# Performance work log

Hardware: AMD Instinct MI355X
Metric: run time of the kernel (lower is better)

The kernel has to match this reference:

```python
import jax, jax.numpy as jnp
import numpy as np

N_WRD = 2000
WCODE = 3
EMB = 32
VSIZE = 7
VIEW = (16, 16)
B = 64
CSIZE = 128


def _vcode():
    # torch.meshgrid with default 'ij' indexing, cat -> (2, H*W) -> (H*W, 2)
    x = jnp.linspace(-1.0, 1.0, VIEW[0])
    y = jnp.linspace(-1.0, 1.0, VIEW[1])
    xg, yg = jnp.meshgrid(x, y, indexing='ij')
    return jnp.stack([xg.reshape(-1), yg.reshape(-1)], axis=-1)  # (V, 2)


def setup_inputs() -> dict:
    key = jax.random.key(0)
    ks = jax.random.split(key, 20)
    s = 0.02
    d = {
        'view_cell': jax.random.normal(ks[0], (B, CSIZE, VIEW[0] * VIEW[1]), jnp.float32),
        'v': jax.random.normal(ks[1], (B, VSIZE), jnp.float32),
        'w2c_w1': jax.random.normal(ks[2], (VSIZE, 512), jnp.float32) * s,
        'w2c_b1': jnp.zeros((512,), jnp.float32),
        'w2c_w2': jax.random.normal(ks[3], (512, WCODE * N_WRD), jnp.float32) * s,
        'w2c_b2': jnp.zeros((WCODE * N_WRD,), jnp.float32),
        'fc1_w': jax.random.normal(ks[4], (WCODE, 256), jnp.float32) * s,
        'fc1_b': jnp.zeros((256,), jnp.float32),
        'fc2_w': jax.random.normal(ks[5], (256, 256), jnp.float32) * s,
        'fc2_b': jnp.zeros((256,), jnp.float32),
        'fca_w': jax.random.normal(ks[6], (256, 1), jnp.float32) * s,
        'fca_b': jnp.zeros((1,), jnp.float32),
        'fce_w': jax.random.normal(ks[7], (256, EMB), jnp.float32) * s,
        'fce_b': jnp.zeros((EMB,), jnp.float32),
        'vse_w1': jax.random.normal(ks[8], (2, 128), jnp.float32) * s,
        'vse_b1': jnp.zeros((128,), jnp.float32),
        'vse_w2': jax.random.normal(ks[9], (128, EMB), jnp.float32) * s,
        'vse_b2': jnp.zeros((EMB,), jnp.float32),
    }
    return d


def reference(view_cell, v, w2c_w1, w2c_b1, w2c_w2, w2c_b2,
              fc1_w, fc1_b, fc2_w, fc2_b, fca_w, fca_b, fce_w, fce_b,
              vse_w1, vse_b1, vse_w2, vse_b2):
    b = v.shape[0]
    # w2c: v -> per-cell world codes
    h0 = jax.nn.relu(v @ w2c_w1 + w2c_b1)                     # (B, 512)
    wcode = (h0 @ w2c_w2 + w2c_b2).reshape(-1, WCODE)          # (B*N, 3)
    h = jax.nn.relu(wcode @ fc1_w + fc1_b)                     # (B*N, 256)
    h = jax.nn.relu(h @ fc2_w + fc2_b)
    activation = jax.nn.sigmoid(h @ fca_w + fca_b).reshape(b, N_WRD, 1)
    cs_emb = (h @ fce_w + fce_b).reshape(b, N_WRD, EMB)        # (B, N, E)
    # view-space embedding of the pixel grid
    vcode = _vcode()                                           # (V, 2)
    vs = jax.nn.relu(vcode @ vse_w1 + vse_b1) @ vse_w2 + vse_b2  # (V, E)
    # relation / gated softmax routing
    relation = jnp.einsum('bne,ve->bnv', cs_emb, vs)           # (B, N, V)
    route = jax.nn.softmax(relation, axis=2) * activation      # (B, N, V)
    # write: view_cell (B, C, V) @ route^T (B, V, N) -> (B, C, N)
    wrd_cell = jnp.einsum('bcv,bnv->bcn', view_cell, route)
    return wrd_cell
```

## Files before the change

### kernel.cpp

```cpp
#include <hip/hip_runtime.h>
#include <hip/hip_bf16.h>
#include <math.h>

#define NWRD 2000

typedef __attribute__((ext_vector_type(8)))  short short8;
typedef __attribute__((ext_vector_type(16))) float f32x16;

#define WS_FC2WT 0
#define WS_WCODE (WS_FC2WT + 32768)
#define WS_VSB   (WS_WCODE + 384000)
#define WS_W2T   (WS_VSB + 4096)
#define WS_VCB   (WS_W2T + 1536000)
#define WS_FCEWT (WS_VCB + 1048576)
#define WS_H0B   (WS_FCEWT + 4096)
#define WS_FCAWB (WS_H0B + 16384)

__device__ __forceinline__ unsigned short f2bf(float x) {
    unsigned int u = __float_as_uint(x);
    u += 0x7fffu + ((u >> 16) & 1u);
    return (unsigned short)(u >> 16);
}
__device__ __forceinline__ unsigned int pkbf(float lo, float hi) {
    unsigned int r;
    asm("v_cvt_pk_bf16_f32 %0, %1, %2" : "=v"(r) : "v"(lo), "v"(hi));
    return r;
}

#define PR_K2  94
#define PR_VCB (PR_K2 + 1024)
#define PR_VSB (PR_VCB + 32)
#define PR_FC2 (PR_VSB + 16)
#define PREP_N (PR_FC2 + 1)
__global__ __launch_bounds__(256) void kprep(
        const float* __restrict__ vc, unsigned short* __restrict__ vcb,
        const float* __restrict__ w2,
        const float* __restrict__ v, const float* __restrict__ w1,
        const float* __restrict__ b1, const float* __restrict__ b2,
        float* __restrict__ wcode,
        const float* __restrict__ vse_w1, const float* __restrict__ vse_b1,
        const float* __restrict__ vse_w2, const float* __restrict__ vse_b2,
        unsigned short* __restrict__ vsb,
        const float* __restrict__ fc2_w, unsigned short* __restrict__ fc2wT,
        const float* __restrict__ fce_w, unsigned short* __restrict__ fcewT,
        const float* __restrict__ fca_w, unsigned short* __restrict__ fcawB) {
    __shared__ __align__(16) unsigned short smem[10240];
    int bid = blockIdx.x, t = threadIdx.x;
    if (bid < PR_K2) {
        unsigned short* ha = smem;
        unsigned short* wb = smem + 4608;
        int n0 = bid * 64;
        int w = t >> 6, lane = t & 63, l31 = lane & 31, h = lane >> 5;
        int mt = w & 1, nt = w >> 1;
        int kk = t & 63, mg = t >> 6;
        int colc = n0 + kk; if (colc > 5999) colc = 5999;
        f32x16 acc;
#pragma unroll
        for (int i = 0; i < 16; i++) acc[i] = 0.f;
        for (int p = 0; p < 8; p++) {
            int k0 = p * 64;
            float w1c[7];
#pragma unroll
            for (int q = 0; q < 7; q++) w1c[q] = w1[q*512 + k0 + kk];
            float bbv = b1[k0 + kk];
#pragma unroll
            for (int mm = 0; mm < 16; mm++) {
                int m = mg*16 + mm;
                float s = bbv;
#pragma unroll
                for (int q = 0; q < 7; q++) s = fmaf(v[m*7 + q], w1c[q], s);
                ha[m*72 + kk] = f2bf(fmaxf(s, 0.f));
            }
#pragma unroll
            for (int i = 0; i < 16; i++)
                wb[kk*72 + mg*16 + i] = f2bf(w2[(size_t)(k0 + mg*16 + i)*6000 + colc]);
            __syncthreads();
#pragma unroll
            for (int ks = 0; ks < 4; ks++) {
                short8 af = *(const short8*)(ha + (mt*32 + l31)*72 + ks*16 + h*8);
                short8 bf = *(const short8*)(wb + (nt*32 + l31)*72 + ks*16 + h*8);
                acc = __builtin_amdgcn_mfma_f32_32x32x16_bf16(af, bf, acc, 0, 0, 0);
            }
            __syncthreads();
        }
        int n = n0 + nt*32 + l31;
        if (n < 6000) {
            float bias = b2[n];
#pragma unroll
            for (int i = 0; i < 16; i++) {
                int row = (i & 3) + 8*(i >> 2) + 4*h;
                wcode[(size_t)(mt*32 + row)*6000 + n] = acc[i] + bias;
            }
        }
    } else if (bid < PR_VCB) {
        int i = ((bid - PR_K2) * 256 + t) * 8;
        float4 f0 = *(const float4*)(vc + i);
        float4 f1 = *(const float4*)(vc + i + 4);
        union { short8 v8; unsigned int u[4]; } o;
        o.u[0] = pkbf(f0.x, f0.y); o.u[1] = pkbf(f0.z, f0.w);
        o.u[2] = pkbf(f1.x, f1.y); o.u[3] = pkbf(f1.z, f1.w);
        *(short8*)(vcb + i) = o.v8;
    } else if (bid < PR_VSB) {
        float* hs = (float*)smem;
        int blk = bid - PR_VCB;
        int m = t & 127, half = t >> 7;
#pragma unroll
        for (int q = 0; q < 4; q++) {
            int vloc = half*4 + q;
            int vv = blk*8 + vloc;
            float x = (2.f/15.f)*(float)(vv >> 4) - 1.f;
            float y = (2.f/15.f)*(float)(vv & 15) - 1.f;
            float hh = vse_b1[m] + x*vse_w1[m] + y*vse_w1[128 + m];
            hs[vloc*128 + m] = fmaxf(hh, 0.f);
        }
        __syncthreads();
        int vloc = t >> 5, e = t & 31;
        float s = vse_b2[e];
        for (int mm = 0; mm < 128; mm++) s = fmaf(hs[vloc*128 + mm], vse_w2[mm*32 + e], s);
        vsb[(blk*8 + vloc)*32 + e] = f2bf(s);
    } else if (bid < PR_FC2) {
        unsigned short (*tile)[72] = (unsigned short(*)[72])smem;
        int b2t = bid - PR_VSB;
        int k0t = (b2t >> 2) * 64, n0t = (b2t & 3) * 64;
        int nl = t & 63, kb = (t >> 6) * 16;
#pragma unroll
        for (int i = 0; i < 16; i++)
            tile[kb + i][nl] = f2bf(fc2_w[(size_t)(k0t + kb + i)*256 + n0t + nl]);
        __syncthreads();
        int kl = t & 63, nb = (t >> 6) * 16;
#pragma unroll
        for (int i = 0; i < 16; i++)
            fc2wT[(size_t)(n0t + nb + i)*256 + k0t + kl] = tile[kl][nb + i];
    } else {
        int e = t & 31, kb = (t >> 5) * 32;
        unsigned short tmp[32];
#pragma unroll
        for (int i = 0; i < 32; i++) tmp[i] = f2bf(fce_w[(size_t)(kb + i)*32 + e]);
#pragma unroll
        for (int i = 0; i < 4; i++)
            *(short8*)(fcewT + (size_t)e*256 + kb + i*8) = *(short8*)(tmp + i*8);
#pragma unroll
        for (int i = 0; i < 32; i++)
            fcawB[(size_t)e*256 + kb + i] = (e == 0) ? f2bf(fca_w[kb + i]) : (unsigned short)0;
    }
}

#define K45_LDS 40192
__global__ __launch_bounds__(512, 4) void k45(
        const unsigned short* __restrict__ vcb,
        const float* __restrict__ wcode,
        const float* __restrict__ fc1_w, const float* __restrict__ fc1_b,
        const unsigned short* __restrict__ fc2wT, const float* __restrict__ fc2_b,
        const float* __restrict__ fca_b_p,
        const unsigned short* __restrict__ fcawB,
        const unsigned short* __restrict__ fcewT, const float* __restrict__ fce_b,
        const unsigned short* __restrict__ vsb,
        float* __restrict__ out) {
    extern __shared__ char lds[];
    unsigned short* buf   = (unsigned short*)lds;
    unsigned short* embL  = (unsigned short*)(lds + 33792);
    float* redS   = (float*)(lds + 38912);
    float* actL   = (float*)(lds + 39936);
    int t = threadIdx.x;
    int w = t >> 6, lane = t & 63, l31 = lane & 31, h = lane >> 5;
    int b = blockIdx.y;
    int n0 = blockIdx.x * 64;

    int jq = (t & 63) * 4;
    int mtF = w & 1, nqF = w >> 1;
    int colA = nqF*64 + l31, colB = colA + 32;
    float baA = fc2_b[colA], baB = fc2_b[colB];
    float be = fce_b[l31];
    float fcab = fca_b_p[0];
    int ntR = w & 1, vq = w >> 1;
    int cq = w >> 1, ntE = w & 1;
    size_t arowE = ((size_t)(b*128 + cq*32 + l31))*256;

    {
        float4 wa  = *(const float4*)(fc1_w + jq);
        float4 wb4 = *(const float4*)(fc1_w + 256 + jq);
        float4 wc  = *(const float4*)(fc1_w + 512 + jq);
        float4 bb4 = *(const float4*)(fc1_b + jq);
        const float* wrow = wcode + (size_t)b*6000;
#pragma unroll
        for (int rr = 0; rr < 8; rr++) {
            int r = w*8 + rr;
            int i = (n0 + r)*3; if (i > 5997) i = 5997;
            float c0 = wrow[i], c1 = wrow[i+1], c2 = wrow[i+2];
            float v0 = fmaxf(fmaf(c2, wc.x, fmaf(c1, wb4.x, fmaf(c0, wa.x, bb4.x))), 0.f);
            float v1 = fmaxf(fmaf(c2, wc.y, fmaf(c1, wb4.y, fmaf(c0, wa.y, bb4.y))), 0.f);
            float v2 = fmaxf(fmaf(c2, wc.z, fmaf(c1, wb4.z, fmaf(c0, wa.z, bb4.z))), 0.f);
            float v3 = fmaxf(fmaf(c2, wc.w, fmaf(c1, wb4.w, fmaf(c0, wa.w, bb4.w))), 0.f);
            uint2 p;
            p.x = pkbf(v0, v1);
            p.y = pkbf(v2, v3);
            *(uint2*)(buf + r*264 + jq) = p;
        }
    }
    __syncthreads();
    f32x16 c0a, c1a;
#pragma unroll
    for (int i = 0; i < 16; i++) { c0a[i] = 0.f; c1a[i] = 0.f; }
#pragma unroll 4
    for (int ks = 0; ks < 16; ks++) {
        int k0 = ks*16 + h*8;
        short8 af  = *(const short8*)(buf + (mtF*32 + l31)*264 + k0);
        short8 bf0 = *(const short8*)(fc2wT + (size_t)colA*256 + k0);
        short8 bf1 = *(const short8*)(fc2wT + (size_t)colB*256 + k0);
        c0a = __builtin_amdgcn_mfma_f32_32x32x16_bf16(af, bf0, c0a, 0, 0, 0);
        c1a = __builtin_amdgcn_mfma_f32_32x32x16_bf16(af, bf1, c1a, 0, 0, 0);
    }
    __syncthreads();
#pragma unroll
    for (int i = 0; i < 16; i++) {
        int row = (i & 3) + 8*(i >> 2) + 4*h;
        unsigned int pk = pkbf(fmaxf(c0a[i] + baA, 0.f), fmaxf(c1a[i] + baB, 0.f));
        buf[(mtF*32 + row)*264 + colA] = (unsigned short)pk;
        buf[(mtF*32 + row)*264 + colB] = (unsigned short)(pk >> 16);
    }
    __syncthreads();
    if (w < 2) {
        f32x16 ce;
#pragma unroll
        for (int i = 0; i < 16; i++) ce[i] = 0.f;
#pragma unroll 4
        for (int ks = 0; ks < 16; ks++) {
            int k0 = ks*16 + h*8;
            short8 af = *(const short8*)(buf + (w*32 + l31)*264 + k0);
            short8 bf = *(const short8*)(fcewT + (size_t)l31*256 + k0);
            ce = __builtin_amdgcn_mfma_f32_32x32x16_bf16(af, bf, ce, 0, 0, 0);
        }
#pragma unroll
        for (int i = 0; i < 16; i += 2) {
            int row = (i & 3) + 8*(i >> 2) + 4*h;
            unsigned int pk = pkbf(ce[i] + be, ce[i+1] + be);
            embL[(w*32 + row)*40 + l31]     = (unsigned short)pk;
            embL[(w*32 + row + 1)*40 + l31] = (unsigned short)(pk >> 16);
        }
    } else if (w < 4) {
        int m = w - 2;
        f32x16 ca;
#pragma unroll
        for (int i = 0; i < 16; i++) ca[i] = 0.f;
#pragma unroll 4
        for (int ks = 0; ks < 16; ks++) {
            int k0 = ks*16 + h*8;
            short8 af = *(const short8*)(buf + (m*32 + l31)*264 + k0);
            short8 bf = *(const short8*)(fcawB + (size_t)l31*256 + k0);
            ca = __builtin_amdgcn_mfma_f32_32x32x16_bf16(af, bf, ca, 0, 0, 0);
        }
        if (l31 == 0) {
#pragma unroll
            for (int i = 0; i < 16; i++) {
                int row = (i & 3) + 8*(i >> 2) + 4*h;
                actL[m*32 + row] = ca[i];
            }
        }
    }
    __syncthreads();
    {
        int nloc = ntR*32 + l31;
        f32x16 ra[2];
#pragma unroll
        for (int mt = 0; mt < 2; mt++)
#pragma unroll
            for (int i = 0; i < 16; i++) ra[mt][i] = 0.f;
#pragma unroll
        for (int s = 0; s < 2; s++) {
            short8 bfrag = *(const short8*)(embL + nloc*40 + s*16 + h*8);
#pragma unroll
            for (int mt = 0; mt < 2; mt++) {
                int vrow = (vq*2 + mt)*32 + l31;
                short8 afrag = *(const short8*)(vsb + vrow*32 + s*16 + h*8);
                ra[mt] = __builtin_amdgcn_mfma_f32_32x32x16_bf16(afrag, bfrag, ra[mt], 0, 0, 0);
            }
        }
        float sm = 0.f;
#pragma unroll
        for (int mt = 0; mt < 2; mt++)
#pragma unroll
            for (int i = 0; i < 16; i++) {
                float e = __expf(ra[mt][i]);
                ra[mt][i] = e;
                sm += e;
            }
        sm += __shfl_xor(sm, 32);
        if (lane < 32) redS[w*32 + l31] = sm;
#pragma unroll
        for (int mt = 0; mt < 2; mt++) {
#pragma unroll
            for (int g = 0; g < 4; g++) {
                int vb = (vq*2 + mt)*32 + 8*g + 4*h;
                unsigned int p0 = pkbf(ra[mt][g*4+0], ra[mt][g*4+1]);
                unsigned int p1 = pkbf(ra[mt][g*4+2], ra[mt][g*4+3]);
                *(uint2*)(buf + nloc*264 + vb) = make_uint2(p0, p1);
            }
        }
    }
    __syncthreads();
    {
        f32x16 cc;
#pragma unroll
        for (int i = 0; i < 16; i++) cc[i] = 0.f;
        const unsigned short* rrow = buf + (ntE*32 + l31)*264;
#pragma unroll 4
        for (int ks = 0; ks < 16; ks++) {
            int k0 = ks*16 + h*8;
            short8 bf = *(const short8*)(rrow + k0);
            short8 a0 = *(const short8*)(vcb + arowE + k0);
            cc = __builtin_amdgcn_mfma_f32_32x32x16_bf16(a0, bf, cc, 0, 0, 0);
        }
        int wloc = ntE*32 + l31;
        float smt = 0.f;
#pragma unroll
        for (int q = 0; q < 4; q++) smt += redS[(q*2 + ntE)*32 + l31];
        float al = actL[wloc] + fcab;
        float scale = (1.f / (1.f + __expf(-al))) / smt;
        int ng = n0 + wloc;
        if (ng < NWRD) {
            float* ob = out + (size_t)b*128*NWRD + ng;
#pragma unroll
            for (int i = 0; i < 16; i++) {
                int crow = (i & 3) + 8*(i >> 2) + 4*h;
                __builtin_nontemporal_store(cc[i]*scale,
                                            ob + (size_t)(cq*32 + crow)*NWRD);
            }
        }
    }
}

extern "C" void kernel_launch(void* const* d_in, const int* in_sizes, int n_in,
                              void* d_out, int out_size, void* d_ws, size_t ws_size,
                              hipStream_t stream) {
    const float* view_cell = (const float*)d_in[0];
    const float* v       = (const float*)d_in[1];
    const float* w2c_w1  = (const float*)d_in[2];
    const float* w2c_b1  = (const float*)d_in[3];
    const float* w2c_w2  = (const float*)d_in[4];
    const float* w2c_b2  = (const float*)d_in[5];
    const float* fc1_w   = (const float*)d_in[6];
    const float* fc1_b   = (const float*)d_in[7];
    const float* fc2_w   = (const float*)d_in[8];
    const float* fc2_b   = (const float*)d_in[9];
    const float* fca_w   = (const float*)d_in[10];
    const float* fca_b   = (const float*)d_in[11];
    const float* fce_w   = (const float*)d_in[12];
    const float* fce_b   = (const float*)d_in[13];
    const float* vse_w1  = (const float*)d_in[14];
    const float* vse_b1  = (const float*)d_in[15];
    const float* vse_w2  = (const float*)d_in[16];
    const float* vse_b2  = (const float*)d_in[17];
    float* ws    = (float*)d_ws;
    unsigned short* fc2wT = (unsigned short*)(ws + WS_FC2WT);
    float* wcode = ws + WS_WCODE;
    unsigned short* vsb   = (unsigned short*)(ws + WS_VSB);
    unsigned short* vcb   = (unsigned short*)(ws + WS_VCB);
    unsigned short* fcewT = (unsigned short*)(ws + WS_FCEWT);
    unsigned short* fcawB = (unsigned short*)(ws + WS_FCAWB);
    float* out   = (float*)d_out;

    kprep<<<PREP_N, 256, 0, stream>>>(view_cell, vcb,
                                      w2c_w2, v, w2c_w1, w2c_b1, w2c_b2, wcode,
                                      vse_w1, vse_b1, vse_w2, vse_b2, vsb,
                                      fc2_w, fc2wT, fce_w, fcewT, fca_w, fcawB);
    (void)hipFuncSetAttribute((const void*)k45,
                              hipFuncAttributeMaxDynamicSharedMemorySize, K45_LDS);
    dim3 g45(32, 64);
    k45<<<g45, 512, K45_LDS, stream>>>(vcb, wcode, fc1_w, fc1_b, fc2wT, fc2_b,
                                       fca_b, fcawB, fcewT, fce_b, vsb, out);
}
```

Before: 235.1 us.

## Double-buffer prep GEMM staging and double k45 block size with 16x16 MFMA splits

The prep w2c GEMM now double-buffers its LDS staging tiles, so the next k-chunk is produced while MFMAs run on the current one. The main fused kernel goes from 512 to 1024 threads per block. Each wave takes a smaller slice of fc2, the embedding/activation heads, the relation softmax and the final write GEMM, with several stages moved to 16x16x32 MFMA tiles. The intent is more waves for latency hiding and better MFMA parallelism in stages that were serialised on a few waves. The cost is a larger prep LDS footprint, a bigger block that may lower occupancy, and more partial-sum reductions for the softmax denominator.

```diff
diff --git a/kernel.cpp b/kernel.cpp
--- a/kernel.cpp
+++ b/kernel.cpp
@@ -6,6 +6,7 @@
 
 typedef __attribute__((ext_vector_type(8)))  short short8;
 typedef __attribute__((ext_vector_type(16))) float f32x16;
+typedef __attribute__((ext_vector_type(4)))  float f32x4v;
 
 #define WS_FC2WT 0
 #define WS_WCODE (WS_FC2WT + 32768)
@@ -44,11 +45,9 @@
         const float* __restrict__ fc2_w, unsigned short* __restrict__ fc2wT,
         const float* __restrict__ fce_w, unsigned short* __restrict__ fcewT,
         const float* __restrict__ fca_w, unsigned short* __restrict__ fcawB) {
-    __shared__ __align__(16) unsigned short smem[10240];
+    __shared__ __align__(16) unsigned short smem[18432];
     int bid = blockIdx.x, t = threadIdx.x;
     if (bid < PR_K2) {
-        unsigned short* ha = smem;
-        unsigned short* wb = smem + 4608;
         int n0 = bid * 64;
         int w = t >> 6, lane = t & 63, l31 = lane & 31, h = lane >> 5;
         int mt = w & 1, nt = w >> 1;
@@ -57,32 +56,42 @@
         f32x16 acc;
 #pragma unroll
         for (int i = 0; i < 16; i++) acc[i] = 0.f;
+#define PRODUCE(p, sel) { \
+        unsigned short* ha = smem + (sel)*9216; \
+        unsigned short* wb = ha + 4608; \
+        int k0 = (p)*64; \
+        float w1c[7]; \
+        _Pragma("unroll") \
+        for (int q = 0; q < 7; q++) w1c[q] = w1[q*512 + k0 + kk]; \
+        float bbv = b1[k0 + kk]; \
+        _Pragma("unroll") \
+        for (int mm = 0; mm < 16; mm++) { \
+            int m = mg*16 + mm; \
+            float s = bbv; \
+            _Pragma("unroll") \
+            for (int q = 0; q < 7; q++) s = fmaf(v[m*7 + q], w1c[q], s); \
+            ha[m*72 + kk] = f2bf(fmaxf(s, 0.f)); \
+        } \
+        _Pragma("unroll") \
+        for (int i = 0; i < 16; i++) \
+            wb[kk*72 + mg*16 + i] = f2bf(w2[(size_t)(k0 + mg*16 + i)*6000 + colc]); }
+        PRODUCE(0, 0)
+        __syncthreads();
         for (int p = 0; p < 8; p++) {
-            int k0 = p * 64;
-            float w1c[7];
-#pragma unroll
-            for (int q = 0; q < 7; q++) w1c[q] = w1[q*512 + k0 + kk];
-            float bbv = b1[k0 + kk];
-#pragma unroll
-            for (int mm = 0; mm < 16; mm++) {
-                int m = mg*16 + mm;
-                float s = bbv;
-#pragma unroll
-                for (int q = 0; q < 7; q++) s = fmaf(v[m*7 + q], w1c[q], s);
-                ha[m*72 + kk] = f2bf(fmaxf(s, 0.f));
-            }
-#pragma unroll
-            for (int i = 0; i < 16; i++)
-                wb[kk*72 + mg*16 + i] = f2bf(w2[(size_t)(k0 + mg*16 + i)*6000 + colc]);
-            __syncthreads();
-#pragma unroll
-            for (int ks = 0; ks < 4; ks++) {
-                short8 af = *(const short8*)(ha + (mt*32 + l31)*72 + ks*16 + h*8);
-                short8 bf = *(const short8*)(wb + (nt*32 + l31)*72 + ks*16 + h*8);
-                acc = __builtin_amdgcn_mfma_f32_32x32x16_bf16(af, bf, acc, 0, 0, 0);
+            if (p < 7) PRODUCE(p + 1, (p + 1) & 1)
+            {
+                unsigned short* ha = smem + (p & 1)*9216;
+                unsigned short* wb = ha + 4608;
+#pragma unroll
+                for (int ks = 0; ks < 4; ks++) {
+                    short8 af = *(const short8*)(ha + (mt*32 + l31)*72 + ks*16 + h*8);
+                    short8 bf = *(const short8*)(wb + (nt*32 + l31)*72 + ks*16 + h*8);
+                    acc = __builtin_amdgcn_mfma_f32_32x32x16_bf16(af, bf, acc, 0, 0, 0);
+                }
             }
             __syncthreads();
         }
+#undef PRODUCE
         int n = n0 + nt*32 + l31;
         if (n < 6000) {
             float bias = b2[n];
@@ -145,8 +154,8 @@
     }
 }
 
-#define K45_LDS 40192
-__global__ __launch_bounds__(512, 4) void k45(
+#define K45_LDS 41216
+__global__ __launch_bounds__(1024, 8) void k45(
         const unsigned short* __restrict__ vcb,
         const float* __restrict__ wcode,
         const float* __restrict__ fc1_w, const float* __restrict__ fc1_b,
@@ -160,31 +169,23 @@
     unsigned short* buf   = (unsigned short*)lds;
     unsigned short* embL  = (unsigned short*)(lds + 33792);
     float* redS   = (float*)(lds + 38912);
-    float* actL   = (float*)(lds + 39936);
+    float* actL   = (float*)(lds + 40960);
     int t = threadIdx.x;
     int w = t >> 6, lane = t & 63, l31 = lane & 31, h = lane >> 5;
+    int l15 = lane & 15, hq = lane >> 4;
     int b = blockIdx.y;
     int n0 = blockIdx.x * 64;
 
-    int jq = (t & 63) * 4;
-    int mtF = w & 1, nqF = w >> 1;
-    int colA = nqF*64 + l31, colB = colA + 32;
-    float baA = fc2_b[colA], baB = fc2_b[colB];
-    float be = fce_b[l31];
-    float fcab = fca_b_p[0];
-    int ntR = w & 1, vq = w >> 1;
-    int cq = w >> 1, ntE = w & 1;
-    size_t arowE = ((size_t)(b*128 + cq*32 + l31))*256;
-
     {
+        int jq = lane * 4;
         float4 wa  = *(const float4*)(fc1_w + jq);
         float4 wb4 = *(const float4*)(fc1_w + 256 + jq);
         float4 wc  = *(const float4*)(fc1_w + 512 + jq);
         float4 bb4 = *(const float4*)(fc1_b + jq);
         const float* wrow = wcode + (size_t)b*6000;
 #pragma unroll
-        for (int rr = 0; rr < 8; rr++) {
-            int r = w*8 + rr;
+        for (int rr = 0; rr < 4; rr++) {
+            int r = w*4 + rr;
             int i = (n0 + r)*3; if (i > 5997) i = 5997;
             float c0 = wrow[i], c1 = wrow[i+1], c2 = wrow[i+2];
             float v0 = fmaxf(fmaf(c2, wc.x, fmaf(c1, wb4.x, fmaf(c0, wa.x, bb4.x))), 0.f);
@@ -198,132 +199,136 @@
         }
     }
     __syncthreads();
-    f32x16 c0a, c1a;
-#pragma unroll
-    for (int i = 0; i < 16; i++) { c0a[i] = 0.f; c1a[i] = 0.f; }
-#pragma unroll 4
-    for (int ks = 0; ks < 16; ks++) {
-        int k0 = ks*16 + h*8;
-        short8 af  = *(const short8*)(buf + (mtF*32 + l31)*264 + k0);
-        short8 bf0 = *(const short8*)(fc2wT + (size_t)colA*256 + k0);
-        short8 bf1 = *(const short8*)(fc2wT + (size_t)colB*256 + k0);
-        c0a = __builtin_amdgcn_mfma_f32_32x32x16_bf16(af, bf0, c0a, 0, 0, 0);
-        c1a = __builtin_amdgcn_mfma_f32_32x32x16_bf16(af, bf1, c1a, 0, 0, 0);
-    }
-    __syncthreads();
-#pragma unroll
-    for (int i = 0; i < 16; i++) {
-        int row = (i & 3) + 8*(i >> 2) + 4*h;
-        unsigned int pk = pkbf(fmaxf(c0a[i] + baA, 0.f), fmaxf(c1a[i] + baB, 0.f));
-        buf[(mtF*32 + row)*264 + colA] = (unsigned short)pk;
-        buf[(mtF*32 + row)*264 + colB] = (unsigned short)(pk >> 16);
-    }
-    __syncthreads();
-    if (w < 2) {
-        f32x16 ce;
-#pragma unroll
-        for (int i = 0; i < 16; i++) ce[i] = 0.f;
+    {
+        int mtF = w & 1;
+        int colF = (w >> 1)*32 + l31;
+        f32x16 acc;
+#pragma unroll
+        for (int i = 0; i < 16; i++) acc[i] = 0.f;
 #pragma unroll 4
         for (int ks = 0; ks < 16; ks++) {
             int k0 = ks*16 + h*8;
-            short8 af = *(const short8*)(buf + (w*32 + l31)*264 + k0);
-            short8 bf = *(const short8*)(fcewT + (size_t)l31*256 + k0);
-            ce = __builtin_amdgcn_mfma_f32_32x32x16_bf16(af, bf, ce, 0, 0, 0);
-        }
-#pragma unroll
-        for (int i = 0; i < 16; i += 2) {
+            short8 af = *(const short8*)(buf + (mtF*32 + l31)*264 + k0);
+            short8 bf = *(const short8*)(fc2wT + (size_t)colF*256 + k0);
+            acc = __builtin_amdgcn_mfma_f32_32x32x16_bf16(af, bf, acc, 0, 0, 0);
+        }
+        __syncthreads();
+        float b2v = fc2_b[colF];
+#pragma unroll
+        for (int i = 0; i < 16; i++) {
             int row = (i & 3) + 8*(i >> 2) + 4*h;
-            unsigned int pk = pkbf(ce[i] + be, ce[i+1] + be);
-            embL[(w*32 + row)*40 + l31]     = (unsigned short)pk;
-            embL[(w*32 + row + 1)*40 + l31] = (unsigned short)(pk >> 16);
-        }
-    } else if (w < 4) {
-        int m = w - 2;
-        f32x16 ca;
-#pragma unroll
-        for (int i = 0; i < 16; i++) ca[i] = 0.f;
+            buf[(mtF*32 + row)*264 + colF] = f2bf(fmaxf(acc[i] + b2v, 0.f));
+        }
+    }
+    __syncthreads();
+    if (w < 8) {
+        int mq = w >> 1, eh = w & 1;
+        f32x4v ce;
+#pragma unroll
+        for (int i = 0; i < 4; i++) ce[i] = 0.f;
 #pragma unroll 4
-        for (int ks = 0; ks < 16; ks++) {
-            int k0 = ks*16 + h*8;
-            short8 af = *(const short8*)(buf + (m*32 + l31)*264 + k0);
-            short8 bf = *(const short8*)(fcawB + (size_t)l31*256 + k0);
-            ca = __builtin_amdgcn_mfma_f32_32x32x16_bf16(af, bf, ca, 0, 0, 0);
-        }
-        if (l31 == 0) {
-#pragma unroll
-            for (int i = 0; i < 16; i++) {
-                int row = (i & 3) + 8*(i >> 2) + 4*h;
-                actL[m*32 + row] = ca[i];
-            }
+        for (int ks = 0; ks < 8; ks++) {
+            int k0 = ks*32 + hq*8;
+            short8 af = *(const short8*)(buf + (mq*16 + l15)*264 + k0);
+            short8 bf = *(const short8*)(fcewT + (size_t)(eh*16 + l15)*256 + k0);
+            ce = __builtin_amdgcn_mfma_f32_16x16x32_bf16(af, bf, ce, 0, 0, 0);
+        }
+        float be2 = fce_b[eh*16 + l15];
+#pragma unroll
+        for (int i = 0; i < 4; i++)
+            embL[(mq*16 + hq*4 + i)*40 + eh*16 + l15] = f2bf(ce[i] + be2);
+    } else if (w < 12) {
+        int mq = w - 8;
+        f32x4v ca;
+#pragma unroll
+        for (int i = 0; i < 4; i++) ca[i] = 0.f;
+#pragma unroll 4
+        for (int ks = 0; ks < 8; ks++) {
+            int k0 = ks*32 + hq*8;
+            short8 af = *(const short8*)(buf + (mq*16 + l15)*264 + k0);
+            short8 bf = *(const short8*)(fcawB + (size_t)l15*256 + k0);
+            ca = __builtin_amdgcn_mfma_f32_16x16x32_bf16(af, bf, ca, 0, 0, 0);
+        }
+        if (l15 == 0) {
+#pragma unroll
+            for (int i = 0; i < 4; i++) actL[mq*16 + hq*4 + i] = ca[i];
         }
     }
     __syncthreads();
     {
-        int nloc = ntR*32 + l31;
-        f32x16 ra[2];
-#pragma unroll
-        for (int mt = 0; mt < 2; mt++)
-#pragma unroll
-            for (int i = 0; i < 16; i++) ra[mt][i] = 0.f;
+        int nloc = (w & 1)*32 + l31;
+        int vq = w >> 1;
+        f32x16 ra;
+#pragma unroll
+        for (int i = 0; i < 16; i++) ra[i] = 0.f;
 #pragma unroll
         for (int s = 0; s < 2; s++) {
+            short8 afrag = *(const short8*)(vsb + (size_t)(vq*32 + l31)*32 + s*16 + h*8);
             short8 bfrag = *(const short8*)(embL + nloc*40 + s*16 + h*8);
-#pragma unroll
-            for (int mt = 0; mt < 2; mt++) {
-                int vrow = (vq*2 + mt)*32 + l31;
-                short8 afrag = *(const short8*)(vsb + vrow*32 + s*16 + h*8);
-                ra[mt] = __builtin_amdgcn_mfma_f32_32x32x16_bf16(afrag, bfrag, ra[mt], 0, 0, 0);
-            }
+            ra = __builtin_amdgcn_mfma_f32_32x32x16_bf16(afrag, bfrag, ra, 0, 0, 0);
         }
         float sm = 0.f;
 #pragma unroll
-        for (int mt = 0; mt < 2; mt++)
-#pragma unroll
-            for (int i = 0; i < 16; i++) {
-                float e = __expf(ra[mt][i]);
-                ra[mt][i] = e;
-                sm += e;
-            }
+        for (int i = 0; i < 16; i++) {
+            float e = __expf(ra[i]);
+            ra[i] = e;
+            sm += e;
+        }
         sm += __shfl_xor(sm, 32);
         if (lane < 32) redS[w*32 + l31] = sm;
 #pragma unroll
-        for (int mt = 0; mt < 2; mt++) {
-#pragma unroll
-            for (int g = 0; g < 4; g++) {
-                int vb = (vq*2 + mt)*32 + 8*g + 4*h;
-                unsigned int p0 = pkbf(ra[mt][g*4+0], ra[mt][g*4+1]);
-                unsigned int p1 = pkbf(ra[mt][g*4+2], ra[mt][g*4+3]);
-                *(uint2*)(buf + nloc*264 + vb) = make_uint2(p0, p1);
-            }
+        for (int g = 0; g < 4; g++) {
+            int vb = vq*32 + 8*g + 4*h;
+            unsigned int p0 = pkbf(ra[g*4+0], ra[g*4+1]);
+            unsigned int p1 = pkbf(ra[g*4+2], ra[g*4+3]);
+            *(uint2*)(buf + nloc*264 + vb) = make_uint2(p0, p1);
         }
     }
     __syncthreads();
     {
-        f32x16 cc;
-#pragma unroll
-        for (int i = 0; i < 16; i++) cc[i] = 0.f;
-        const unsigned short* rrow = buf + (ntE*32 + l31)*264;
+        int cg = w >> 1, nh = w & 1;
+        f32x4v p0, p1;
+#pragma unroll
+        for (int i = 0; i < 4; i++) { p0[i] = 0.f; p1[i] = 0.f; }
+        size_t arow = ((size_t)(b*128 + cg*16 + l15))*256;
+        const unsigned short* r0 = buf + (nh*32 + l15)*264;
+        const unsigned short* r1 = r0 + 16*264;
 #pragma unroll 4
-        for (int ks = 0; ks < 16; ks++) {
-            int k0 = ks*16 + h*8;
-            short8 bf = *(const short8*)(rrow + k0);
-            short8 a0 = *(const short8*)(vcb + arowE + k0);
-            cc = __builtin_amdgcn_mfma_f32_32x32x16_bf16(a0, bf, cc, 0, 0, 0);
-        }
-        int wloc = ntE*32 + l31;
-        float smt = 0.f;
-#pragma unroll
-        for (int q = 0; q < 4; q++) smt += redS[(q*2 + ntE)*32 + l31];
-        float al = actL[wloc] + fcab;
-        float scale = (1.f / (1.f + __expf(-al))) / smt;
-        int ng = n0 + wloc;
-        if (ng < NWRD) {
-            float* ob = out + (size_t)b*128*NWRD + ng;
-#pragma unroll
-            for (int i = 0; i < 16; i++) {
-                int crow = (i & 3) + 8*(i >> 2) + 4*h;
-                __builtin_nontemporal_store(cc[i]*scale,
-                                            ob + (size_t)(cq*32 + crow)*NWRD);
+        for (int ks = 0; ks < 8; ks++) {
+            int k0 = ks*32 + hq*8;
+            short8 af  = *(const short8*)(vcb + arow + k0);
+            short8 bf0 = *(const short8*)(r0 + k0);
+            short8 bf1 = *(const short8*)(r1 + k0);
+            p0 = __builtin_amdgcn_mfma_f32_16x16x32_bf16(af, bf0, p0, 0, 0, 0);
+            p1 = __builtin_amdgcn_mfma_f32_16x16x32_bf16(af, bf1, p1, 0, 0, 0);
+        }
+        float fcab = fca_b_p[0];
+        float* ob = out + (size_t)b*128*NWRD;
+        int crow = cg*16 + hq*4;
+        {
+            int nl = nh*32 + l15;
+            float smt = 0.f;
+#pragma unroll
+            for (int q = 0; q < 8; q++) smt += redS[(q*2 + nh)*32 + (nl & 31)];
+            float scale = (1.f / (1.f + __expf(-(actL[nl] + fcab)))) / smt;
+            int ng = n0 + nl;
+            if (ng < NWRD) {
+#pragma unroll
+                for (int i = 0; i < 4; i++)
+                    __builtin_nontemporal_store(p0[i]*scale, ob + (size_t)(crow + i)*NWRD + ng);
+            }
+        }
+        {
+            int nl = nh*32 + 16 + l15;
+            float smt = 0.f;
+#pragma unroll
+            for (int q = 0; q < 8; q++) smt += redS[(q*2 + nh)*32 + (nl & 31)];
+            float scale = (1.f / (1.f + __expf(-(actL[nl] + fcab)))) / smt;
+            int ng = n0 + nl;
+            if (ng < NWRD) {
+#pragma unroll
+                for (int i = 0; i < 4; i++)
+                    __builtin_nontemporal_store(p1[i]*scale, ob + (size_t)(crow + i)*NWRD + ng);
             }
         }
     }
@@ -366,6 +371,6 @@
     (void)hipFuncSetAttribute((const void*)k45,
                               hipFuncAttributeMaxDynamicSharedMemorySize, K45_LDS);
     dim3 g45(32, 64);
-    k45<<<g45, 512, K45_LDS, stream>>>(vcb, wcode, fc1_w, fc1_b, fc2wT, fc2_b,
-                                       fca_b, fcawB, fcewT, fce_b, vsb, out);
-}
+    k45<<<g45, 1024, K45_LDS, stream>>>(vcb, wcode, fc1_w, fc1_b, fc2wT, fc2_b,
+                                        fca_b, fcawB, fcewT, fce_b, vsb, out);
+}
```

After: 257.3 us. 9.4% more time.
